# Performance work log

Measured on AMD Instinct MI355X. Metric: run time of the kernel, lower is better.

The kernel has to match this reference:

```python
import jax, jax.numpy as jnp
import numpy as np

# dims
B, L, HID, TDIM, LT = 8, 4096, 1024, 768, 77
DIM = 512            # vmamba_dim
D_INNER = 2 * DIM    # expand = 2
NHEADS = DIM // 16   # 32
HEADDIM = D_INNER // NHEADS  # 32
D_STATE = 64
CONV_K = 4
CONV_DIM = D_INNER + 2 * D_STATE  # 1152
D_PROJ = 2 * D_INNER + 2 * D_STATE + NHEADS  # z | xBC | dt


def setup_inputs() -> dict:
    key = jax.random.key(0)
    ks = jax.random.split(key, 20)
    s = 0.02
    return {
        "image_tokens": jax.random.normal(ks[0], (B, L, HID), jnp.float32),
        "text_tokens": jax.random.normal(ks[1], (B, LT, TDIM), jnp.float32),
        "W_in": jax.random.normal(ks[2], (HID, DIM), jnp.float32) * s,
        "b_in": jnp.zeros((DIM,), jnp.float32),
        "W_txt": jax.random.normal(ks[3], (TDIM, DIM), jnp.float32) * s,
        "b_txt": jnp.zeros((DIM,), jnp.float32),
        "norm_w": jnp.ones((DIM,), jnp.float32),
        "norm_b": jnp.zeros((DIM,), jnp.float32),
        "W_zxbcdt": jax.random.normal(ks[4], (DIM, D_PROJ), jnp.float32) * s,
        "b_zxbcdt": jnp.zeros((D_PROJ,), jnp.float32),
        "conv_w": jax.random.normal(ks[5], (CONV_DIM, CONV_K), jnp.float32) * 0.1,
        "conv_b": jnp.zeros((CONV_DIM,), jnp.float32),
        "dt_bias": jax.random.uniform(ks[6], (NHEADS,), jnp.float32, -4.0, -2.0),
        "A_log": jnp.log(jnp.arange(1, NHEADS + 1, dtype=jnp.float32)),
        "D": jnp.ones((NHEADS,), jnp.float32),
        "W_blk_out": jax.random.normal(ks[7], (D_INNER, DIM), jnp.float32) * s,
        "b_blk_out": jnp.zeros((DIM,), jnp.float32),
        "W_out": jax.random.normal(ks[8], (DIM, HID), jnp.float32) * s,
        "b_out": jnp.zeros((HID,), jnp.float32),
    }


def _layernorm(x, w, b, eps=1e-5):
    mu = x.mean(-1, keepdims=True)
    var = ((x - mu) ** 2).mean(-1, keepdims=True)
    return (x - mu) * jax.lax.rsqrt(var + eps) * w + b


def _mamba2_block(tok, norm_w, norm_b, W_zxbcdt, b_zxbcdt, conv_w, conv_b,
                  dt_bias, A_log, Dp, W_blk_out, b_blk_out):
    x = _layernorm(tok, norm_w, norm_b)
    zxbcdt = x @ W_zxbcdt + b_zxbcdt                       # [B,L,D_PROJ]
    z = zxbcdt[..., :D_INNER]
    xBC = zxbcdt[..., D_INNER:D_INNER + CONV_DIM]
    dt = zxbcdt[..., D_INNER + CONV_DIM:]                  # [B,L,H]
    # causal depthwise conv1d, kernel 4
    xp = jnp.pad(xBC, ((0, 0), (CONV_K - 1, 0), (0, 0)))
    conv = sum(xp[:, k:k + L, :] * conv_w[None, None, :, k] for k in range(CONV_K))
    xBC = jax.nn.silu(conv + conv_b)
    xh = xBC[..., :D_INNER].reshape(B, L, NHEADS, HEADDIM)  # [B,L,H,P]
    Bm = xBC[..., D_INNER:D_INNER + D_STATE]                # [B,L,N]
    Cm = xBC[..., D_INNER + D_STATE:]                       # [B,L,N]
    dt = jax.nn.softplus(dt + dt_bias)                      # [B,L,H]
    A = -jnp.exp(A_log)                                     # [H]
    dA = jnp.exp(dt * A)                                    # [B,L,H]

    def step(h, xs):
        dA_t, dt_t, B_t, C_t, x_t = xs   # [B,H],[B,H],[B,N],[B,N],[B,H,P]
        h = h * dA_t[:, :, None, None] + \
            (dt_t[:, :, None, None] * x_t[..., None]) * B_t[:, None, None, :]
        y = jnp.einsum('bhpn,bn->bhp', h, C_t)
        return h, y

    xs = (dA.transpose(1, 0, 2), dt.transpose(1, 0, 2),
          Bm.transpose(1, 0, 2), Cm.transpose(1, 0, 2),
          xh.transpose(1, 0, 2, 3))
    h0 = jnp.zeros((B, NHEADS, HEADDIM, D_STATE), tok.dtype)
    _, ys = jax.lax.scan(step, h0, xs)                      # [L,B,H,P]
    y = ys.transpose(1, 0, 2, 3) + Dp[None, None, :, None] * xh
    y = y.reshape(B, L, D_INNER) * jax.nn.silu(z)
    return tok + (y @ W_blk_out + b_blk_out)                # residual


def reference(image_tokens, text_tokens, W_in, b_in, W_txt, b_txt,
              norm_w, norm_b, W_zxbcdt, b_zxbcdt, conv_w, conv_b,
              dt_bias, A_log, D, W_blk_out, b_blk_out, W_out, b_out):
    txt = text_tokens[:, 0, :] @ W_txt + b_txt              # cls pool
    tok = image_tokens @ W_in + b_in + txt[:, None, :]
    tok = _mamba2_block(tok, norm_w, norm_b, W_zxbcdt, b_zxbcdt, conv_w,
                        conv_b, dt_bias, A_log, D, W_blk_out, b_blk_out)
    tok = tok @ W_out + b_out                               # [B,L,HID]
    return tok.mean(axis=1)                                 # AdaptiveAvgPool1d(1)
```

## Files before the change

kernel.cpp:

```cpp
#include <hip/hip_runtime.h>

typedef unsigned short U16;
typedef __attribute__((ext_vector_type(4))) float f32x4;
typedef __attribute__((ext_vector_type(8))) short short8;
typedef __attribute__((ext_vector_type(8))) __bf16 bf16x8;

#define Bsz 8
#define Lsz 4096
#define HID 1024
#define DIMV 512
#define D_INNER 1024
#define NHEADS 32
#define HEADDIM 32
#define D_STATE 64
#define CONV_DIM 1152
#define D_PROJ 2208
#define D_PROJ_PAD 2304
#define MROWS 32768
#define CL2 256
#define NSUB 4
#define NCH 16

__device__ __forceinline__ float bf2f(U16 u) {
  return __builtin_bit_cast(float, (unsigned)(((unsigned)u) << 16));
}
__device__ __forceinline__ U16 f2bf(float f) {
  unsigned u = __builtin_bit_cast(unsigned, f);
  return (U16)((u + 0x7FFFu + ((u >> 16) & 1u)) >> 16);
}
__device__ __forceinline__ void gload_lds16(const void* g, void* l) {
  __builtin_amdgcn_global_load_lds((const __attribute__((address_space(1))) unsigned int*)g,
                                   (__attribute__((address_space(3))) unsigned int*)l, 16, 0, 0);
}

__global__ __launch_bounds__(512) void txt_kernel(const float* __restrict__ text,
                                                  const float* __restrict__ Wt,
                                                  const float* __restrict__ bt,
                                                  float* __restrict__ txt) {
  int b = blockIdx.x, j = threadIdx.x;
  float s = bt[j];
  const float* tp = text + (size_t)b * 77 * 768;
  for (int k = 0; k < 768; ++k) s += tp[k] * Wt[(size_t)k * 512 + j];
  txt[b * 512 + j] = s;
}

__global__ __launch_bounds__(256) void transpose_cvt_kernel(const float* __restrict__ in,
                                                            U16* __restrict__ out,
                                                            int K, int N, int Npad) {
  __shared__ U16 tile[32][33];
  int n0 = blockIdx.x * 32, k0 = blockIdx.y * 32;
  int tx = threadIdx.x, ty = threadIdx.y;
  #pragma unroll
  for (int i = 0; i < 4; ++i) {
    int k = k0 + ty + i * 8, n = n0 + tx;
    float v = (n < N) ? in[(size_t)k * N + n] : 0.f;
    tile[ty + i * 8][tx] = f2bf(v);
  }
  __syncthreads();
  #pragma unroll
  for (int i = 0; i < 4; ++i) {
    int n = n0 + ty + i * 8;
    out[(size_t)n * K + k0 + tx] = tile[tx][ty + i * 8];
  }
}

template <int EPI, int AF32, int TRANS>
__global__ __launch_bounds__(256) void gemm_kernel(const void* __restrict__ Ap,
                                                   const U16* __restrict__ Bt,
                                                   U16* __restrict__ C,
                                                   const float* __restrict__ bias,
                                                   const float* __restrict__ txtv,
                                                   int M, int K, int Nreal, int NT) {
  __shared__ alignas(16) U16 smem[128 * 128];
  U16* As = smem;
  U16* Bs = smem + 128 * 64;
  const int tid = threadIdx.x;
  const int wid = tid >> 6, lane = tid & 63;
  const int lhi = lane >> 4, llo = lane & 15;
  const int xcd = blockIdx.x & 7, slot = blockIdx.x >> 3;
  const int m0 = (xcd + 8 * (slot / NT)) * 128;
  const int n0 = (slot % NT) * 128;
  const int wr = wid >> 1, wc = wid & 1;
  f32x4 acc[4][4] = {};

  for (int k0 = 0; k0 < K; k0 += 64) {
    __syncthreads();
    if constexpr (AF32) {
      const float* Af = (const float*)Ap;
      #pragma unroll
      for (int is = 0; is < 4; ++is) {
        int q = is * 256 + tid;
        int r = q >> 3, cl = q & 7;
        int cg = cl ^ (r & 7);
        const float* src = Af + (size_t)(m0 + r) * K + k0 + cg * 8;
        f32x4 v0 = *reinterpret_cast<const f32x4*>(src);
        f32x4 v1 = *reinterpret_cast<const f32x4*>(src + 4);
        short8 o;
        #pragma unroll
        for (int j = 0; j < 4; ++j) {
          o[j] = (short)f2bf(v0[j]);
          o[j + 4] = (short)f2bf(v1[j]);
        }
        *reinterpret_cast<short8*>(&As[q * 8]) = o;
      }
    } else {
      const U16* A = (const U16*)Ap;
      #pragma unroll
      for (int is = 0; is < 4; ++is) {
        int qbase = is * 256 + wid * 64;
        int q = qbase + lane;
        int r = q >> 3;
        int cc = (q & 7) ^ (r & 7);
        gload_lds16(A + (size_t)(m0 + r) * K + k0 + cc * 8, &As[qbase * 8]);
      }
    }
    #pragma unroll
    for (int is = 0; is < 4; ++is) {
      int qbase = is * 256 + wid * 64;
      int q = qbase + lane;
      int r = q >> 3;
      int cc = (q & 7) ^ (r & 7);
      gload_lds16(Bt + (size_t)(n0 + r) * K + k0 + cc * 8, &Bs[qbase * 8]);
    }
    __syncthreads();
    #pragma unroll
    for (int kk = 0; kk < 64; kk += 32) {
      bf16x8 av[4], bv[4];
      #pragma unroll
      for (int i = 0; i < 4; ++i) {
        int ra = wr * 64 + i * 16 + llo;
        short8 a = *reinterpret_cast<const short8*>(
            &As[ra * 64 + ((((kk >> 3) + lhi) ^ (ra & 7)) << 3)]);
        av[i] = __builtin_bit_cast(bf16x8, a);
        int rb = wc * 64 + i * 16 + llo;
        short8 b = *reinterpret_cast<const short8*>(
            &Bs[rb * 64 + ((((kk >> 3) + lhi) ^ (rb & 7)) << 3)]);
        bv[i] = __builtin_bit_cast(bf16x8, b);
      }
      #pragma unroll
      for (int i = 0; i < 4; ++i)
        #pragma unroll
        for (int j = 0; j < 4; ++j)
          acc[i][j] = __builtin_amdgcn_mfma_f32_16x16x32_bf16(av[i], bv[j], acc[i][j], 0, 0, 0);
    }
  }
  const int b = m0 >> 12;
  if constexpr (TRANS) {
    __syncthreads();
    U16* T = smem;
    #pragma unroll
    for (int i = 0; i < 4; ++i) {
      #pragma unroll
      for (int j = 0; j < 4; ++j) {
        int c_loc = wc * 64 + j * 16 + llo;
        int cg = n0 + c_loc;
        float badd = (cg < D_PROJ) ? bias[cg] : 0.f;
        int q = wr * 16 + i * 4 + lhi;
        int qs = q ^ ((c_loc & 15) << 1);
        U16 pk[4];
        #pragma unroll
        for (int r = 0; r < 4; ++r) {
          float v = acc[i][j][r] + badd;
          if (cg < 1024) v = v / (1.f + __expf(-v));
          pk[r] = f2bf(v);
        }
        uint2 p2;
        p2.x = (unsigned)pk[0] | ((unsigned)pk[1] << 16);
        p2.y = (unsigned)pk[2] | ((unsigned)pk[3] << 16);
        *reinterpret_cast<uint2*>(&T[c_loc * 128 + qs * 4]) = p2;
      }
    }
    __syncthreads();
    const int l0 = m0 & 4095;
    #pragma unroll
    for (int cs = 0; cs < 8; ++cs) {
      int c = cs * 16 + (tid >> 4);
      int gch = n0 + c;
      int kp = (tid & 15) * 2;
      int q0 = kp ^ ((c & 15) << 1);
      int q1 = (kp + 1) ^ ((c & 15) << 1);
      uint2 a = *reinterpret_cast<const uint2*>(&T[c * 128 + q0 * 4]);
      uint2 bq = *reinterpret_cast<const uint2*>(&T[c * 128 + q1 * 4]);
      if (gch < D_PROJ) {
        uint4 oo;
        oo.x = a.x; oo.y = a.y; oo.z = bq.x; oo.w = bq.y;
        *reinterpret_cast<uint4*>(C + ((size_t)b * D_PROJ_PAD + gch) * 4096 + l0 + kp * 4) = oo;
      }
    }
  } else {
    #pragma unroll
    for (int i = 0; i < 4; ++i) {
      int rbase = m0 + wr * 64 + i * 16 + lhi * 4;
      #pragma unroll
      for (int j = 0; j < 4; ++j) {
        int cg = n0 + wc * 64 + j * 16 + llo;
        if (cg < Nreal) {
          float badd = bias[cg] + (EPI ? txtv[b * 512 + cg] : 0.f);
          #pragma unroll
          for (int r = 0; r < 4; ++r)
            C[(size_t)(rbase + r) * Nreal + cg] = f2bf(acc[i][j][r] + badd);
        }
      }
    }
  }
}

__global__ __launch_bounds__(128) void ln_kernel(const U16* __restrict__ tok,
                                                 U16* __restrict__ xo,
                                                 const float* __restrict__ w,
                                                 const float* __restrict__ bb) {
  int row = blockIdx.x, tid = threadIdx.x;
  const U16* rp = tok + (size_t)row * 512 + tid * 4;
  uint2 raw = *reinterpret_cast<const uint2*>(rp);
  float f0 = bf2f((U16)(raw.x & 0xffff)), f1 = bf2f((U16)(raw.x >> 16));
  float f2 = bf2f((U16)(raw.y & 0xffff)), f3 = bf2f((U16)(raw.y >> 16));
  float s = f0 + f1 + f2 + f3;
  float q = f0 * f0 + f1 * f1 + f2 * f2 + f3 * f3;
  for (int m = 1; m < 64; m <<= 1) { s += __shfl_xor(s, m); q += __shfl_xor(q, m); }
  __shared__ float ss[2], qq[2];
  if ((tid & 63) == 0) { ss[tid >> 6] = s; qq[tid >> 6] = q; }
  __syncthreads();
  s = ss[0] + ss[1]; q = qq[0] + qq[1];
  float mu = s * (1.f / 512.f);
  float var = q * (1.f / 512.f) - mu * mu;
  float rs = rsqrtf(var + 1e-5f);
  int j0 = tid * 4;
  unsigned c0 = f2bf((f0 - mu) * rs * w[j0] + bb[j0]);
  unsigned c1 = f2bf((f1 - mu) * rs * w[j0 + 1] + bb[j0 + 1]);
  unsigned c2 = f2bf((f2 - mu) * rs * w[j0 + 2] + bb[j0 + 2]);
  unsigned c3 = f2bf((f3 - mu) * rs * w[j0 + 3] + bb[j0 + 3]);
  uint2 o; o.x = c0 | (c1 << 16); o.y = c2 | (c3 << 16);
  *reinterpret_cast<uint2*>(xo + (size_t)row * 512 + j0) = o;
}

__global__ __launch_bounds__(256) void tokpart_kernel(const U16* __restrict__ tok,
                                                      float* __restrict__ part) {
  int b = blockIdx.x, j = blockIdx.y * 256 + threadIdx.x, z = blockIdx.z;
  float s = 0.f;
  int l0 = z * 256;
  for (int l = l0; l < l0 + 256; ++l)
    s += bf2f(tok[((size_t)b * Lsz + l) * 512 + j]);
  part[(z * 8 + b) * 512 + j] = s;
}

__global__ __launch_bounds__(256) void decay_kernel(const U16* __restrict__ zxT,
                                                    const float* __restrict__ dt_bias,
                                                    const float* __restrict__ A_log,
                                                    float* __restrict__ decay4) {
  const int sc = blockIdx.x;
  const int w = threadIdx.x >> 6, l = threadIdx.x & 63;
  const int r0 = sc * 64;
  const int b = r0 >> 12, l0 = r0 & 4095;
  #pragma unroll
  for (int i = 0; i < 8; ++i) {
    int hh = w * 8 + i;
    float raw = bf2f(zxT[((size_t)b * D_PROJ_PAD + 2176 + hh) * 4096 + l0 + l]) + dt_bias[hh];
    float dt = (raw > 20.f) ? raw : log1pf(__expf(raw));
    float A = -__expf(A_log[hh]);
    float ldA2 = dt * A * 1.44269504088896f;
    float ldt2 = __log2f(dt);
    float la = ldA2;
    #pragma unroll
    for (int d = 1; d < 64; d <<= 1) {
      float o = __shfl_up(la, d);
      if (l >= d) la += o;
    }
    float laend = __shfl(la, 63);
    f32x4 v = {ldt2 - la, la, exp2f(la), exp2f(laend + ldt2 - la)};
    *reinterpret_cast<f32x4*>(decay4 + ((size_t)(b * 32 + hh) * 4096 + l0 + l) * 4) = v;
  }
}

__global__ __launch_bounds__(256) void conv_t_kernel(
    const U16* __restrict__ zxT, const float* __restrict__ cw,
    const float* __restrict__ cb, U16* __restrict__ xh_t,
    U16* __restrict__ bm_t, U16* __restrict__ cm_t,
    U16* __restrict__ Bmo, U16* __restrict__ Cmo) {
  __shared__ U16 Tc[64 * 264];
  const int lc = blockIdx.x, cg = blockIdx.y, b = blockIdx.z;
  const int tid = threadIdx.x;
  const int cl = tid & 63, ls = tid >> 6;
  const int cc2 = cg * 64 + cl;
  const int l0 = lc * 256 + ls * 64;
  const U16* row = zxT + ((size_t)b * D_PROJ_PAD + 1024 + cc2) * 4096;

  U16 arr[72];
  {
    const U16* src = row + l0 - 8;
    #pragma unroll
    for (int k = 0; k < 9; ++k) {
      uint4 rv;
      if (l0 == 0 && k == 0) {
        rv.x = rv.y = rv.z = rv.w = 0u;
      } else {
        rv = *reinterpret_cast<const uint4*>(src + k * 8);
      }
      arr[k * 8 + 0] = (U16)(rv.x & 0xffff); arr[k * 8 + 1] = (U16)(rv.x >> 16);
      arr[k * 8 + 2] = (U16)(rv.y & 0xffff); arr[k * 8 + 3] = (U16)(rv.y >> 16);
      arr[k * 8 + 4] = (U16)(rv.z & 0xffff); arr[k * 8 + 5] = (U16)(rv.z >> 16);
      arr[k * 8 + 6] = (U16)(rv.w & 0xffff); arr[k * 8 + 7] = (U16)(rv.w >> 16);
    }
  }
  const float4 w4 = *reinterpret_cast<const float4*>(cw + cc2 * 4);
  const float cbv = cb[cc2];
  U16 o[64];
  #pragma unroll
  for (int j = 0; j < 64; ++j) {
    float acc = cbv + bf2f(arr[j + 5]) * w4.x + bf2f(arr[j + 6]) * w4.y +
                bf2f(arr[j + 7]) * w4.z + bf2f(arr[j + 8]) * w4.w;
    o[j] = f2bf(acc / (1.f + __expf(-acc)));
  }
  {
    U16* dst;
    if (cc2 < 1024)      dst = xh_t + ((size_t)b * 1024 + cc2) * 4096 + l0;
    else if (cc2 < 1088) dst = bm_t + ((size_t)(b * 64 + (cc2 - 1024))) * 4096 + l0;
    else                 dst = cm_t + ((size_t)(b * 64 + (cc2 - 1088))) * 4096 + l0;
    #pragma unroll
    for (int k = 0; k < 8; ++k) {
      uint4 ov;
      ov.x = (unsigned)o[k * 8 + 0] | ((unsigned)o[k * 8 + 1] << 16);
      ov.y = (unsigned)o[k * 8 + 2] | ((unsigned)o[k * 8 + 3] << 16);
      ov.z = (unsigned)o[k * 8 + 4] | ((unsigned)o[k * 8 + 5] << 16);
      ov.w = (unsigned)o[k * 8 + 6] | ((unsigned)o[k * 8 + 7] << 16);
      *reinterpret_cast<uint4*>(dst + k * 8) = ov;
    }
  }
  if (cg >= 16) {
    #pragma unroll
    for (int k = 0; k < 8; ++k) {
      uint4 ov;
      ov.x = (unsigned)o[k * 8 + 0] | ((unsigned)o[k * 8 + 1] << 16);
      ov.y = (unsigned)o[k * 8 + 2] | ((unsigned)o[k * 8 + 3] << 16);
      ov.z = (unsigned)o[k * 8 + 4] | ((unsigned)o[k * 8 + 5] << 16);
      ov.w = (unsigned)o[k * 8 + 6] | ((unsigned)o[k * 8 + 7] << 16);
      *reinterpret_cast<uint4*>(&Tc[cl * 264 + ls * 64 + k * 8]) = ov;
    }
    __syncthreads();
    U16* outp = (cg == 16) ? Bmo : Cmo;
    const int lt = tid;
    U16 rowv[64];
    #pragma unroll
    for (int n = 0; n < 64; ++n) rowv[n] = Tc[n * 264 + lt];
    U16* dst = outp + ((size_t)b * 4096 + lc * 256 + lt) * 64;
    #pragma unroll
    for (int k = 0; k < 8; ++k) {
      uint4 ov;
      ov.x = (unsigned)rowv[k * 8 + 0] | ((unsigned)rowv[k * 8 + 1] << 16);
      ov.y = (unsigned)rowv[k * 8 + 2] | ((unsigned)rowv[k * 8 + 3] << 16);
      ov.z = (unsigned)rowv[k * 8 + 4] | ((unsigned)rowv[k * 8 + 5] << 16);
      ov.w = (unsigned)rowv[k * 8 + 6] | ((unsigned)rowv[k * 8 + 7] << 16);
      *reinterpret_cast<uint4*>(dst + k * 8) = ov;
    }
  }
}

__global__ __launch_bounds__(256, 2) void scan_chunk_kernel(
    const U16* __restrict__ xh_t, const U16* __restrict__ zxT,
    const U16* __restrict__ Bm, const U16* __restrict__ Cm,
    const U16* __restrict__ bm_t, const U16* __restrict__ cm_t,
    const float* __restrict__ decay4, const float* __restrict__ Dp,
    U16* __restrict__ hpart, U16* __restrict__ wacc,
    float* __restrict__ ylocal, float* __restrict__ aprod) {
  const int w = threadIdx.x >> 6, l = threadIdx.x & 63;
  const int bid = (blockIdx.x & 7) * 128 + (blockIdx.x >> 3);
  const int u = bid * 4 + w;
  const int hh = u & 31, ci = (u >> 5) & (NCH - 1), b = u >> 9;
  const int tl = l & 15, lg = l >> 4;

  __shared__ alignas(16) U16 MsmAll[4 * 64 * 72];
  __shared__ alignas(16) float decAll[4 * 256];
  U16* Msm = &MsmAll[w * 64 * 72];
  float* qsm = &decAll[w * 256];
  float* la2sm = qsm + 64;
  float* casm = qsm + 128;
  float* cfsm = qsm + 192;

  #pragma unroll
  for (int i = 0; i < 9; ++i)
    *reinterpret_cast<f32x4*>(reinterpret_cast<char*>(Msm) + (size_t)l * 144 + i * 16) =
        f32x4{0.f, 0.f, 0.f, 0.f};

  f32x4 hC[2][4] = {};
  f32x4 WB[2][4] = {};
  f32x4 corrp[2] = {};
  float ylac[2] = {0.f, 0.f}, dxac[2] = {0.f, 0.f};
  float capfx = 1.f;
  const size_t xrow = ((size_t)b * 1024 + hh * 32) * 4096;
  const size_t grow = ((size_t)b * D_PROJ_PAD + hh * 32) * 4096;
  const float* dbase = decay4 + ((size_t)(b * 32 + hh) * 4096) * 4;

  for (int sc = 0; sc < NSUB; ++sc) {
    const int lglob = ci * CL2 + sc * 64;
    const int r0g = b * 4096 + lglob;

    f32x4 dv = *reinterpret_cast<const f32x4*>(dbase + (size_t)(lglob + l) * 4);
    qsm[l] = dv[0];
    la2sm[l] = dv[1];
    casm[l] = dv[2];
    cfsm[l] = dv[3];
    const float cs = __shfl(dv[2], 63);

    short8 graw[2][2], xraw[2][2];
    #pragma unroll
    for (int pt = 0; pt < 2; ++pt)
      #pragma unroll
      for (int kt = 0; kt < 2; ++kt) {
        size_t po = (size_t)(pt * 16 + tl) * 4096 + lglob + kt * 32 + lg * 8;
        graw[pt][kt] = *reinterpret_cast<const short8*>(zxT + grow + po);
        xraw[pt][kt] = *reinterpret_cast<const short8*>(xh_t + xrow + po);
      }

    {
      f32x4 g[7] = {};
      #pragma unroll
      for (int k = 0; k < 2; ++k) {
        const size_t co = (size_t)k * 32 + lg * 8;
        bf16x8 af0 = *reinterpret_cast<const bf16x8*>(Bm + (size_t)(r0g + tl) * 64 + co);
        bf16x8 af1 = *reinterpret_cast<const bf16x8*>(Bm + (size_t)(r0g + 16 + tl) * 64 + co);
        bf16x8 cf0 = *reinterpret_cast<const bf16x8*>(Cm + (size_t)(r0g + tl) * 64 + co);
        bf16x8 cf1 = *reinterpret_cast<const bf16x8*>(Cm + (size_t)(r0g + 16 + tl) * 64 + co);
        bf16x8 cf2 = *reinterpret_cast<const bf16x8*>(Cm + (size_t)(r0g + 32 + tl) * 64 + co);
        bf16x8 cf3 = *reinterpret_cast<const bf16x8*>(Cm + (size_t)(r0g + 48 + tl) * 64 + co);
        __builtin_amdgcn_s_setprio(1);
        g[0] = __builtin_amdgcn_mfma_f32_16x16x32_bf16(af0, cf0, g[0], 0, 0, 0);
        g[1] = __builtin_amdgcn_mfma_f32_16x16x32_bf16(af0, cf1, g[1], 0, 0, 0);
        g[2] = __builtin_amdgcn_mfma_f32_16x16x32_bf16(af0, cf2, g[2], 0, 0, 0);
        g[3] = __builtin_amdgcn_mfma_f32_16x16x32_bf16(af0, cf3, g[3], 0, 0, 0);
        g[4] = __builtin_amdgcn_mfma_f32_16x16x32_bf16(af1, cf1, g[4], 0, 0, 0);
        g[5] = __builtin_amdgcn_mfma_f32_16x16x32_bf16(af1, cf2, g[5], 0, 0, 0);
        g[6] = __builtin_amdgcn_mfma_f32_16x16x32_bf16(af1, cf3, g[6], 0, 0, 0);
        __builtin_amdgcn_s_setprio(0);
      }
      f32x4 q0 = *reinterpret_cast<const f32x4*>(&qsm[lg * 4]);
      f32x4 q1 = *reinterpret_cast<const f32x4*>(&qsm[16 + lg * 4]);
      #pragma unroll
      for (int idx = 0; idx < 7; ++idx) {
        const int si = (idx < 4) ? 0 : 1;
        const int ti = (idx < 4) ? idx : (idx - 3);
        f32x4 q4 = si ? q1 : q0;
        float lat = la2sm[ti * 16 + tl];
        float v[4];
        #pragma unroll
        for (int r = 0; r < 4; ++r) {
          float val = g[idx][r] * exp2f(lat + q4[r]);
          if (si == ti) val = (lg * 4 + r <= tl) ? val : 0.f;
          v[r] = val;
        }
        uint2 pk;
        pk.x = (unsigned)f2bf(v[0]) | ((unsigned)f2bf(v[1]) << 16);
        pk.y = (unsigned)f2bf(v[2]) | ((unsigned)f2bf(v[3]) << 16);
        *reinterpret_cast<uint2*>(reinterpret_cast<char*>(Msm) +
                                  (size_t)(ti * 16 + tl) * 144 + (size_t)(si * 16 + lg * 4) * 2) = pk;
      }
    }
    {
      f32x4 g[3] = {};
      #pragma unroll
      for (int k = 0; k < 2; ++k) {
        const size_t co = (size_t)k * 32 + lg * 8;
        bf16x8 af2 = *reinterpret_cast<const bf16x8*>(Bm + (size_t)(r0g + 32 + tl) * 64 + co);
        bf16x8 af3 = *reinterpret_cast<const bf16x8*>(Bm + (size_t)(r0g + 48 + tl) * 64 + co);
        bf16x8 cf2 = *reinterpret_cast<const bf16x8*>(Cm + (size_t)(r0g + 32 + tl) * 64 + co);
        bf16x8 cf3 = *reinterpret_cast<const bf16x8*>(Cm + (size_t)(r0g + 48 + tl) * 64 + co);
        __builtin_amdgcn_s_setprio(1);
        g[0] = __builtin_amdgcn_mfma_f32_16x16x32_bf16(af2, cf2, g[0], 0, 0, 0);
        g[1] = __builtin_amdgcn_mfma_f32_16x16x32_bf16(af2, cf3, g[1], 0, 0, 0);
        g[2] = __builtin_amdgcn_mfma_f32_16x16x32_bf16(af3, cf3, g[2], 0, 0, 0);
        __builtin_amdgcn_s_setprio(0);
      }
      f32x4 q2 = *reinterpret_cast<const f32x4*>(&qsm[32 + lg * 4]);
      f32x4 q3 = *reinterpret_cast<const f32x4*>(&qsm[48 + lg * 4]);
      const int sis[3] = {2, 2, 3};
      const int tis[3] = {2, 3, 3};
      #pragma unroll
      for (int idx = 0; idx < 3; ++idx) {
        const int si = sis[idx], ti = tis[idx];
        f32x4 q4 = (si == 2) ? q2 : q3;
        float lat = la2sm[ti * 16 + tl];
        float v[4];
        #pragma unroll
        for (int r = 0; r < 4; ++r) {
          float val = g[idx][r] * exp2f(lat + q4[r]);
          if (si == ti) val = (lg * 4 + r <= tl) ? val : 0.f;
          v[r] = val;
        }
        uint2 pk;
        pk.x = (unsigned)f2bf(v[0]) | ((unsigned)f2bf(v[1]) << 16);
        pk.y = (unsigned)f2bf(v[2]) | ((unsigned)f2bf(v[3]) << 16);
        *reinterpret_cast<uint2*>(reinterpret_cast<char*>(Msm) +
                                  (size_t)(ti * 16 + tl) * 144 + (size_t)(si * 16 + lg * 4) * 2) = pk;
      }
    }

    bf16x8 ga[2][2], xa[2][2];
    #pragma unroll
    for (int pt = 0; pt < 2; ++pt)
      #pragma unroll
      for (int kt = 0; kt < 2; ++kt) {
        const float* cap = &casm[kt * 32 + lg * 8];
        const float* cfp = &cfsm[kt * 32 + lg * 8];
        short8 gs, xs8;
        #pragma unroll
        for (int j = 0; j < 8; ++j) {
          float gf = bf2f((U16)graw[pt][kt][j]);
          float xf = bf2f((U16)xraw[pt][kt][j]);
          dxac[pt] = fmaf(gf, xf, dxac[pt]);
          gs[j] = (short)f2bf(gf * cap[j]);
          xs8[j] = (short)f2bf(xf * cfp[j]);
        }
        ga[pt][kt] = __builtin_bit_cast(bf16x8, gs);
        xa[pt][kt] = __builtin_bit_cast(bf16x8, xs8);
      }

    {
      uint2 gzp[4][2];
      #pragma unroll
      for (int tt = 0; tt < 4; ++tt)
        #pragma unroll
        for (int pt = 0; pt < 2; ++pt)
          gzp[tt][pt] = *reinterpret_cast<const uint2*>(
              zxT + grow + (size_t)(pt * 16 + tl) * 4096 + lglob + tt * 16 + lg * 4);
      #pragma unroll
      for (int tt = 0; tt < 4; ++tt) {
        f32x4 y[2] = {f32x4{0.f, 0.f, 0.f, 0.f}, f32x4{0.f, 0.f, 0.f, 0.f}};
        __builtin_amdgcn_s_setprio(1);
        #pragma unroll
        for (int ks = 0; ks < 2; ++ks) {
          bf16x8 mf = *reinterpret_cast<const bf16x8*>(
              reinterpret_cast<char*>(Msm) + (size_t)(tt * 16 + tl) * 144 + (ks * 32 + lg * 8) * 2);
          #pragma unroll
          for (int pt = 0; pt < 2; ++pt)
            y[pt] = __builtin_amdgcn_mfma_f32_16x16x32_bf16(
                mf, __builtin_bit_cast(bf16x8, xraw[pt][ks]), y[pt], 0, 0, 0);
        }
        __builtin_amdgcn_s_setprio(0);
        #pragma unroll
        for (int pt = 0; pt < 2; ++pt) {
          uint2 gz2 = gzp[tt][pt];
          float gzv[4] = {bf2f((U16)(gz2.x & 0xffff)), bf2f((U16)(gz2.x >> 16)),
                          bf2f((U16)(gz2.y & 0xffff)), bf2f((U16)(gz2.y >> 16))};
          #pragma unroll
          for (int r = 0; r < 4; ++r)
            ylac[pt] = fmaf(gzv[r], y[pt][r], ylac[pt]);
        }
      }
    }

    #pragma unroll
    for (int nt = 0; nt < 4; ++nt) {
      size_t cro = (size_t)(b * 64 + nt * 16 + tl) * 4096 + lglob;
      bf16x8 cb0 = *reinterpret_cast<const bf16x8*>(cm_t + cro + lg * 8);
      bf16x8 cb1 = *reinterpret_cast<const bf16x8*>(cm_t + cro + 32 + lg * 8);
      bf16x8 bb0 = *reinterpret_cast<const bf16x8*>(bm_t + cro + lg * 8);
      bf16x8 bb1 = *reinterpret_cast<const bf16x8*>(bm_t + cro + 32 + lg * 8);
      __builtin_amdgcn_s_setprio(1);
      #pragma unroll
      for (int pt = 0; pt < 2; ++pt) {
        f32x4 z4 = {0.f, 0.f, 0.f, 0.f};
        f32x4 ws = __builtin_amdgcn_mfma_f32_16x16x32_bf16(ga[pt][0], cb0, z4, 0, 0, 0);
        ws = __builtin_amdgcn_mfma_f32_16x16x32_bf16(ga[pt][1], cb1, ws, 0, 0, 0);
        f32x4 hs = __builtin_amdgcn_mfma_f32_16x16x32_bf16(xa[pt][0], bb0, z4, 0, 0, 0);
        hs = __builtin_amdgcn_mfma_f32_16x16x32_bf16(xa[pt][1], bb1, hs, 0, 0, 0);
        corrp[pt] = corrp[pt] + hC[pt][nt] * ws;
        WB[pt][nt] = WB[pt][nt] + ws * capfx;
        hC[pt][nt] = hC[pt][nt] * cs + hs;
      }
      __builtin_amdgcn_s_setprio(0);
    }
    capfx *= cs;
  }

  #pragma unroll
  for (int pt = 0; pt < 2; ++pt)
    #pragma unroll
    for (int nt = 0; nt < 4; ++nt) {
      size_t slot = (size_t)u * 2048 + (size_t)((pt * 4 + nt) * 64 + l) * 4;
      ushort4 hp, wp;
      hp.x = f2bf(hC[pt][nt][0]); hp.y = f2bf(hC[pt][nt][1]);
      hp.z = f2bf(hC[pt][nt][2]); hp.w = f2bf(hC[pt][nt][3]);
      wp.x = f2bf(WB[pt][nt][0]); wp.y = f2bf(WB[pt][nt][1]);
      wp.z = f2bf(WB[pt][nt][2]); wp.w = f2bf(WB[pt][nt][3]);
      *reinterpret_cast<ushort4*>(hpart + slot) = hp;
      *reinterpret_cast<ushort4*>(wacc + slot) = wp;
    }
  float corrv[2][4];
  #pragma unroll
  for (int pt = 0; pt < 2; ++pt)
    #pragma unroll
    for (int r = 0; r < 4; ++r) {
      float c = corrp[pt][r];
      c += __shfl_xor(c, 1); c += __shfl_xor(c, 2);
      c += __shfl_xor(c, 4); c += __shfl_xor(c, 8);
      corrv[pt][r] = c;
    }
  const float Dh = Dp[hh];
  float* ysm = qsm;
  #pragma unroll
  for (int pt = 0; pt < 2; ++pt) {
    float yv = ylac[pt] + Dh * dxac[pt];
    yv += __shfl_xor(yv, 16);
    yv += __shfl_xor(yv, 32);
    if (l < 16) ysm[pt * 16 + l] = yv;
  }
  if (tl == 0) {
    #pragma unroll
    for (int pt = 0; pt < 2; ++pt)
      #pragma unroll
      for (int r = 0; r < 4; ++r)
        ysm[pt * 16 + lg * 4 + r] += corrv[pt][r];
  }
  if (l < 32) ylocal[(size_t)u * 32 + l] = ysm[l];
  if (l == 0) aprod[u] = capfx;
}

__global__ __launch_bounds__(256) void scan_combine_kernel(
    const U16* __restrict__ hpart, const U16* __restrict__ wacc,
    const float* __restrict__ ylocal, const float* __restrict__ aprod,
    float* __restrict__ yysum) {
  const int bh = blockIdx.x;
  const int b = bh >> 5, hh = bh & 31;
  const int w = threadIdx.x >> 6, l = threadIdx.x & 63;
  const int tl = l & 15, lg = l >> 4;
  __shared__ float csm[8][16];
  __shared__ float ylsm[32];
  const int pair0 = w * 2;
  f32x4 hr[2] = {};
  float cv[2][4] = {};
  for (int ci = 0; ci < NCH; ++ci) {
    int bx = (b * NCH + ci) * 32 + hh;
    size_t base = (size_t)bx * 2048 + (size_t)l * 4;
    float ap = aprod[bx];
    #pragma unroll
    for (int k = 0; k < 2; ++k) {
      size_t o = base + (size_t)(pair0 + k) * 256;
      ushort4 wraw = *reinterpret_cast<const ushort4*>(wacc + o);
      ushort4 praw = *reinterpret_cast<const ushort4*>(hpart + o);
      f32x4 wv = {bf2f(wraw.x), bf2f(wraw.y), bf2f(wraw.z), bf2f(wraw.w)};
      f32x4 pv = {bf2f(praw.x), bf2f(praw.y), bf2f(praw.z), bf2f(praw.w)};
      f32x4 a4 = hr[k] * wv;
      #pragma unroll
      for (int r = 0; r < 4; ++r) cv[k][r] += a4[r];
      hr[k] = hr[k] * ap + pv;
    }
  }
  #pragma unroll
  for (int k = 0; k < 2; ++k)
    #pragma unroll
    for (int r = 0; r < 4; ++r) {
      float c = cv[k][r];
      c += __shfl_xor(c, 1); c += __shfl_xor(c, 2);
      c += __shfl_xor(c, 4); c += __shfl_xor(c, 8);
      if (tl == 0) csm[pair0 + k][lg * 4 + r] = c;
    }
  if (threadIdx.x < 32) {
    float yl = 0.f;
    for (int ci = 0; ci < NCH; ++ci)
      yl += ylocal[(size_t)((b * NCH + ci) * 32 + hh) * 32 + threadIdx.x];
    ylsm[threadIdx.x] = yl;
  }
  __syncthreads();
  if (threadIdx.x < 32) {
    int p = threadIdx.x;
    int pt = p >> 4, pl = p & 15;
    float corr = csm[pt * 4 + 0][pl] + csm[pt * 4 + 1][pl] +
                 csm[pt * 4 + 2][pl] + csm[pt * 4 + 3][pl];
    yysum[(size_t)b * 1024 + hh * 32 + p] = ylsm[p] + corr;
  }
}

__global__ __launch_bounds__(128) void final1_kernel(const float* __restrict__ tokpart,
                                                     const float* __restrict__ yysum,
                                                     const float* __restrict__ Wb,
                                                     const float* __restrict__ bb,
                                                     float* __restrict__ m2) {
  int b = blockIdx.x, j = blockIdx.y * 128 + threadIdx.x;
  float tm = 0.f;
  #pragma unroll
  for (int z = 0; z < 16; ++z) tm += tokpart[(z * 8 + b) * 512 + j];
  float s = 0.f;
  for (int d = 0; d < 1024; ++d) s += yysum[b * 1024 + d] * Wb[(size_t)d * 512 + j];
  m2[b * 512 + j] = (tm + s) * (1.f / (float)Lsz) + bb[j];
}

__global__ __launch_bounds__(256) void final2_kernel(const float* __restrict__ m2,
                                                     const float* __restrict__ Wo,
                                                     const float* __restrict__ bo,
                                                     float* __restrict__ out) {
  int b = blockIdx.x, o = blockIdx.y * 256 + threadIdx.x;
  float s = 0.f;
  for (int j = 0; j < 512; ++j) s += m2[b * 512 + j] * Wo[(size_t)j * 1024 + o];
  out[b * 1024 + o] = s + bo[o];
}

extern "C" void kernel_launch(void* const* d_in, const int* in_sizes, int n_in,
                              void* d_out, int out_size, void* d_ws, size_t ws_size,
                              hipStream_t stream) {
  const float* image = (const float*)d_in[0];
  const float* text = (const float*)d_in[1];
  const float* W_in = (const float*)d_in[2];
  const float* b_in = (const float*)d_in[3];
  const float* W_txt = (const float*)d_in[4];
  const float* b_txt = (const float*)d_in[5];
  const float* norm_w = (const float*)d_in[6];
  const float* norm_b = (const float*)d_in[7];
  const float* W_zx = (const float*)d_in[8];
  const float* b_zx = (const float*)d_in[9];
  const float* conv_w = (const float*)d_in[10];
  const float* conv_b = (const float*)d_in[11];
  const float* dt_bias = (const float*)d_in[12];
  const float* A_log = (const float*)d_in[13];
  const float* Dp = (const float*)d_in[14];
  const float* W_blk = (const float*)d_in[15];
  const float* b_blk = (const float*)d_in[16];
  const float* W_out = (const float*)d_in[17];
  const float* b_out = (const float*)d_in[18];
  float* out = (float*)d_out;

  char* ws = (char*)d_ws;
  size_t off = 0;
  auto take = [&](size_t bytes) {
    char* p = ws + off;
    off = (off + bytes + 255) & ~(size_t)255;
    return p;
  };
  U16* zxT = (U16*)take((size_t)Bsz * D_PROJ_PAD * 4096 * 2);
  U16* wt_in = (U16*)take((size_t)DIMV * HID * 2);
  U16* wt_zx = (U16*)take((size_t)D_PROJ_PAD * DIMV * 2);
  U16* tok_bf = (U16*)take((size_t)MROWS * DIMV * 2);
  U16* x_bf = (U16*)take((size_t)MROWS * DIMV * 2);
  U16* xh_t = (U16*)take((size_t)MROWS * D_INNER * 2);
  U16* bm_bf = (U16*)take((size_t)MROWS * 64 * 2);
  U16* cm_bf = (U16*)take((size_t)MROWS * 64 * 2);
  U16* bm_t = (U16*)take((size_t)MROWS * 64 * 2);
  U16* cm_t = (U16*)take((size_t)MROWS * 64 * 2);
  float* decay4 = (float*)take((size_t)256 * 4096 * 16);
  float* txtf = (float*)take(8 * 512 * 4);
  float* tokpart = (float*)take(16 * 8 * 512 * 4);
  float* yysum = (float*)take(8 * 1024 * 4);
  float* m2 = (float*)take(8 * 512 * 4);
  float* ylocal = (float*)take((size_t)4096 * 32 * 4);
  float* aprod = (float*)take((size_t)4096 * 4);
  U16* hpart = tok_bf;
  U16* wacc = x_bf;

  txt_kernel<<<8, 512, 0, stream>>>(text, W_txt, b_txt, txtf);
  transpose_cvt_kernel<<<dim3(DIMV / 32, HID / 32), dim3(32, 8), 0, stream>>>(W_in, wt_in, HID, DIMV, DIMV);
  transpose_cvt_kernel<<<dim3(D_PROJ_PAD / 32, DIMV / 32), dim3(32, 8), 0, stream>>>(W_zx, wt_zx, DIMV, D_PROJ, D_PROJ_PAD);

  gemm_kernel<1, 1, 0><<<1024, 256, 0, stream>>>(
      (const void*)image, wt_in, tok_bf, b_in, txtf, MROWS, HID, DIMV, 4);
  tokpart_kernel<<<dim3(8, 2, 16), 256, 0, stream>>>(tok_bf, tokpart);
  ln_kernel<<<MROWS, 128, 0, stream>>>(tok_bf, x_bf, norm_w, norm_b);

  gemm_kernel<0, 0, 1><<<4608, 256, 0, stream>>>(
      (const void*)x_bf, wt_zx, zxT, b_zx, nullptr, MROWS, DIMV, D_PROJ, 18);

  decay_kernel<<<512, 256, 0, stream>>>(zxT, dt_bias, A_log, decay4);
  conv_t_kernel<<<dim3(16, 18, 8), 256, 0, stream>>>(zxT, conv_w, conv_b,
                                                     xh_t, bm_t, cm_t, bm_bf, cm_bf);

  scan_chunk_kernel<<<1024, 256, 0, stream>>>(xh_t, zxT, bm_bf, cm_bf, bm_t, cm_t,
                                              decay4, Dp, hpart, wacc, ylocal, aprod);
  scan_combine_kernel<<<256, 256, 0, stream>>>(hpart, wacc, ylocal, aprod, yysum);

  final1_kernel<<<dim3(8, 4), 128, 0, stream>>>(tokpart, yysum, W_blk, b_blk, m2);
  final2_kernel<<<dim3(8, 4), 256, 0, stream>>>(m2, W_out, b_out, out);
}
```

Measured before the change: 537.4 us.

## Fuse token column sums into input GEMM epilogue, use fast SiLU, hoist gate loads

Removes the separate tokpart reduction kernel. The first GEMM's epilogue now accumulates per-tile column sums of the fp32 token values and writes them to a colp buffer, which final1 reduces over 32 tiles per batch. SiLU now uses a hardware reciprocal instead of a division in the GEMM and conv kernels, and the scan kernel issues its gate loads earlier so they overlap the MFMA work. Column sums are taken before bf16 rounding, which slightly changes numerics. The extra shuffles, barriers and registers add a little epilogue cost.

```diff
diff --git a/kernel.cpp b/kernel.cpp
--- a/kernel.cpp
+++ b/kernel.cpp
@@ -32,6 +32,9 @@
   __builtin_amdgcn_global_load_lds((const __attribute__((address_space(1))) unsigned int*)g,
                                    (__attribute__((address_space(3))) unsigned int*)l, 16, 0, 0);
 }
+__device__ __forceinline__ float fast_silu(float v) {
+  return v * __builtin_amdgcn_rcpf(1.f + __expf(-v));
+}
 
 __global__ __launch_bounds__(512) void txt_kernel(const float* __restrict__ text,
                                                   const float* __restrict__ Wt,
@@ -70,6 +73,7 @@
                                                    U16* __restrict__ C,
                                                    const float* __restrict__ bias,
                                                    const float* __restrict__ txtv,
+                                                   float* __restrict__ colp,
                                                    int M, int K, int Nreal, int NT) {
   __shared__ alignas(16) U16 smem[128 * 128];
   U16* As = smem;
@@ -161,7 +165,7 @@
         #pragma unroll
         for (int r = 0; r < 4; ++r) {
           float v = acc[i][j][r] + badd;
-          if (cg < 1024) v = v / (1.f + __expf(-v));
+          if (cg < 1024) v = fast_silu(v);
           pk[r] = f2bf(v);
         }
         uint2 p2;
@@ -188,6 +192,7 @@
       }
     }
   } else {
+    float cp[4] = {0.f, 0.f, 0.f, 0.f};
     #pragma unroll
     for (int i = 0; i < 4; ++i) {
       int rbase = m0 + wr * 64 + i * 16 + lhi * 4;
@@ -197,10 +202,30 @@
         if (cg < Nreal) {
           float badd = bias[cg] + (EPI ? txtv[b * 512 + cg] : 0.f);
           #pragma unroll
-          for (int r = 0; r < 4; ++r)
-            C[(size_t)(rbase + r) * Nreal + cg] = f2bf(acc[i][j][r] + badd);
+          for (int r = 0; r < 4; ++r) {
+            float v = acc[i][j][r] + badd;
+            C[(size_t)(rbase + r) * Nreal + cg] = f2bf(v);
+            if constexpr (EPI) cp[j] += v;
+          }
         }
       }
+    }
+    if constexpr (EPI) {
+      #pragma unroll
+      for (int j = 0; j < 4; ++j) {
+        cp[j] += __shfl_xor(cp[j], 16);
+        cp[j] += __shfl_xor(cp[j], 32);
+      }
+      __syncthreads();
+      float* colsm = reinterpret_cast<float*>(smem);
+      if (lane < 16) {
+        #pragma unroll
+        for (int j = 0; j < 4; ++j)
+          colsm[wr * 128 + wc * 64 + j * 16 + lane] = cp[j];
+      }
+      __syncthreads();
+      if (tid < 128)
+        colp[(size_t)(m0 >> 7) * 512 + n0 + tid] = colsm[tid] + colsm[128 + tid];
     }
   }
 }
@@ -233,16 +258,6 @@
   *reinterpret_cast<uint2*>(xo + (size_t)row * 512 + j0) = o;
 }
 
-__global__ __launch_bounds__(256) void tokpart_kernel(const U16* __restrict__ tok,
-                                                      float* __restrict__ part) {
-  int b = blockIdx.x, j = blockIdx.y * 256 + threadIdx.x, z = blockIdx.z;
-  float s = 0.f;
-  int l0 = z * 256;
-  for (int l = l0; l < l0 + 256; ++l)
-    s += bf2f(tok[((size_t)b * Lsz + l) * 512 + j]);
-  part[(z * 8 + b) * 512 + j] = s;
-}
-
 __global__ __launch_bounds__(256) void decay_kernel(const U16* __restrict__ zxT,
                                                     const float* __restrict__ dt_bias,
                                                     const float* __restrict__ A_log,
@@ -308,7 +323,7 @@
   for (int j = 0; j < 64; ++j) {
     float acc = cbv + bf2f(arr[j + 5]) * w4.x + bf2f(arr[j + 6]) * w4.y +
                 bf2f(arr[j + 7]) * w4.z + bf2f(arr[j + 8]) * w4.w;
-    o[j] = f2bf(acc / (1.f + __expf(-acc)));
+    o[j] = f2bf(fast_silu(acc));
   }
   {
     U16* dst;
@@ -401,6 +416,7 @@
     const float cs = __shfl(dv[2], 63);
 
     short8 graw[2][2], xraw[2][2];
+    uint2 gzp[4][2];
     #pragma unroll
     for (int pt = 0; pt < 2; ++pt)
       #pragma unroll
@@ -409,6 +425,12 @@
         graw[pt][kt] = *reinterpret_cast<const short8*>(zxT + grow + po);
         xraw[pt][kt] = *reinterpret_cast<const short8*>(xh_t + xrow + po);
       }
+    #pragma unroll
+    for (int tt = 0; tt < 4; ++tt)
+      #pragma unroll
+      for (int pt = 0; pt < 2; ++pt)
+        gzp[tt][pt] = *reinterpret_cast<const uint2*>(
+            zxT + grow + (size_t)(pt * 16 + tl) * 4096 + lglob + tt * 16 + lg * 4);
 
     {
       f32x4 g[7] = {};
@@ -512,37 +534,28 @@
         xa[pt][kt] = __builtin_bit_cast(bf16x8, xs8);
       }
 
-    {
-      uint2 gzp[4][2];
-      #pragma unroll
-      for (int tt = 0; tt < 4; ++tt)
+    #pragma unroll
+    for (int tt = 0; tt < 4; ++tt) {
+      f32x4 y[2] = {f32x4{0.f, 0.f, 0.f, 0.f}, f32x4{0.f, 0.f, 0.f, 0.f}};
+      __builtin_amdgcn_s_setprio(1);
+      #pragma unroll
+      for (int ks = 0; ks < 2; ++ks) {
+        bf16x8 mf = *reinterpret_cast<const bf16x8*>(
+            reinterpret_cast<char*>(Msm) + (size_t)(tt * 16 + tl) * 144 + (ks * 32 + lg * 8) * 2);
         #pragma unroll
         for (int pt = 0; pt < 2; ++pt)
-          gzp[tt][pt] = *reinterpret_cast<const uint2*>(
-              zxT + grow + (size_t)(pt * 16 + tl) * 4096 + lglob + tt * 16 + lg * 4);
-      #pragma unroll
-      for (int tt = 0; tt < 4; ++tt) {
-        f32x4 y[2] = {f32x4{0.f, 0.f, 0.f, 0.f}, f32x4{0.f, 0.f, 0.f, 0.f}};
-        __builtin_amdgcn_s_setprio(1);
-        #pragma unroll
-        for (int ks = 0; ks < 2; ++ks) {
-          bf16x8 mf = *reinterpret_cast<const bf16x8*>(
-              reinterpret_cast<char*>(Msm) + (size_t)(tt * 16 + tl) * 144 + (ks * 32 + lg * 8) * 2);
-          #pragma unroll
-          for (int pt = 0; pt < 2; ++pt)
-            y[pt] = __builtin_amdgcn_mfma_f32_16x16x32_bf16(
-                mf, __builtin_bit_cast(bf16x8, xraw[pt][ks]), y[pt], 0, 0, 0);
-        }
-        __builtin_amdgcn_s_setprio(0);
-        #pragma unroll
-        for (int pt = 0; pt < 2; ++pt) {
-          uint2 gz2 = gzp[tt][pt];
-          float gzv[4] = {bf2f((U16)(gz2.x & 0xffff)), bf2f((U16)(gz2.x >> 16)),
-                          bf2f((U16)(gz2.y & 0xffff)), bf2f((U16)(gz2.y >> 16))};
-          #pragma unroll
-          for (int r = 0; r < 4; ++r)
-            ylac[pt] = fmaf(gzv[r], y[pt][r], ylac[pt]);
-        }
+          y[pt] = __builtin_amdgcn_mfma_f32_16x16x32_bf16(
+              mf, __builtin_bit_cast(bf16x8, xraw[pt][ks]), y[pt], 0, 0, 0);
+      }
+      __builtin_amdgcn_s_setprio(0);
+      #pragma unroll
+      for (int pt = 0; pt < 2; ++pt) {
+        uint2 gz2 = gzp[tt][pt];
+        float gzv[4] = {bf2f((U16)(gz2.x & 0xffff)), bf2f((U16)(gz2.x >> 16)),
+                        bf2f((U16)(gz2.y & 0xffff)), bf2f((U16)(gz2.y >> 16))};
+        #pragma unroll
+        for (int r = 0; r < 4; ++r)
+          ylac[pt] = fmaf(gzv[r], y[pt][r], ylac[pt]);
       }
     }
 
@@ -668,7 +681,7 @@
   }
 }
 
-__global__ __launch_bounds__(128) void final1_kernel(const float* __restrict__ tokpart,
+__global__ __launch_bounds__(128) void final1_kernel(const float* __restrict__ colp,
                                                      const float* __restrict__ yysum,
                                                      const float* __restrict__ Wb,
                                                      const float* __restrict__ bb,
@@ -676,7 +689,7 @@
   int b = blockIdx.x, j = blockIdx.y * 128 + threadIdx.x;
   float tm = 0.f;
   #pragma unroll
-  for (int z = 0; z < 16; ++z) tm += tokpart[(z * 8 + b) * 512 + j];
+  for (int t = 0; t < 32; ++t) tm += colp[(size_t)(b * 32 + t) * 512 + j];
   float s = 0.f;
   for (int d = 0; d < 1024; ++d) s += yysum[b * 1024 + d] * Wb[(size_t)d * 512 + j];
   m2[b * 512 + j] = (tm + s) * (1.f / (float)Lsz) + bb[j];
@@ -735,7 +748,7 @@
   U16* cm_t = (U16*)take((size_t)MROWS * 64 * 2);
   float* decay4 = (float*)take((size_t)256 * 4096 * 16);
   float* txtf = (float*)take(8 * 512 * 4);
-  float* tokpart = (float*)take(16 * 8 * 512 * 4);
+  float* colp = (float*)take((size_t)256 * 512 * 4);
   float* yysum = (float*)take(8 * 1024 * 4);
   float* m2 = (float*)take(8 * 512 * 4);
   float* ylocal = (float*)take((size_t)4096 * 32 * 4);
@@ -748,12 +761,11 @@
   transpose_cvt_kernel<<<dim3(D_PROJ_PAD / 32, DIMV / 32), dim3(32, 8), 0, stream>>>(W_zx, wt_zx, DIMV, D_PROJ, D_PROJ_PAD);
 
   gemm_kernel<1, 1, 0><<<1024, 256, 0, stream>>>(
-      (const void*)image, wt_in, tok_bf, b_in, txtf, MROWS, HID, DIMV, 4);
-  tokpart_kernel<<<dim3(8, 2, 16), 256, 0, stream>>>(tok_bf, tokpart);
+      (const void*)image, wt_in, tok_bf, b_in, txtf, colp, MROWS, HID, DIMV, 4);
   ln_kernel<<<MROWS, 128, 0, stream>>>(tok_bf, x_bf, norm_w, norm_b);
 
   gemm_kernel<0, 0, 1><<<4608, 256, 0, stream>>>(
-      (const void*)x_bf, wt_zx, zxT, b_zx, nullptr, MROWS, DIMV, D_PROJ, 18);
+      (const void*)x_bf, wt_zx, zxT, b_zx, nullptr, nullptr, MROWS, DIMV, D_PROJ, 18);
 
   decay_kernel<<<512, 256, 0, stream>>>(zxT, dt_bias, A_log, decay4);
   conv_t_kernel<<<dim3(16, 18, 8), 256, 0, stream>>>(zxT, conv_w, conv_b,
@@ -763,6 +775,6 @@
                                               decay4, Dp, hpart, wacc, ylocal, aprod);
   scan_combine_kernel<<<256, 256, 0, stream>>>(hpart, wacc, ylocal, aprod, yysum);
 
-  final1_kernel<<<dim3(8, 4), 128, 0, stream>>>(tokpart, yysum, W_blk, b_blk, m2);
+  final1_kernel<<<dim3(8, 4), 128, 0, stream>>>(colp, yysum, W_blk, b_blk, m2);
   final2_kernel<<<dim3(8, 4), 256, 0, stream>>>(m2, W_out, b_out, out);
 }
```

Measured after the change: 534.0 us. No clear change (-0.6%).
